# Kernel tuning notes

Measured on AMD Instinct MI355X. Metric: run time of the kernel, lower is better.

## Reference

```python
import jax, jax.numpy as jnp
import numpy as np

N, M, CIN, COUT, K, KS = 200000, 100000, 32, 64, 32, 3


def setup_inputs() -> dict:
    key = jax.random.key(0)
    ks = jax.random.split(key, 6)
    inp_positions = jax.random.uniform(ks[0], (N, 3), dtype=jnp.float32)
    out_positions = jax.random.uniform(ks[1], (M, 3), dtype=jnp.float32)
    inp_features = jax.random.normal(ks[2], (N, CIN), dtype=jnp.float32)
    inp_importance = jnp.ones((N,), dtype=jnp.float32)
    neighbors_index = jax.random.randint(ks[3], (M, K), 0, N, dtype=jnp.int32)
    kernel = 0.05 * jax.random.normal(ks[4], (KS, KS, KS, CIN, COUT), dtype=jnp.float32)
    bias = jnp.zeros((COUT,), dtype=jnp.float32)
    extents = jnp.ones((1,), dtype=jnp.float32)
    return dict(inp_features=inp_features, inp_positions=inp_positions,
                out_positions=out_positions, extents=extents,
                inp_importance=inp_importance, neighbors_index=neighbors_index,
                kernel=kernel, bias=bias)


def _axis_weights(x):
    """x: [...,] coord clamped to [0, KS-1]. Returns [..., KS] linear interp weights."""
    grid = jnp.arange(KS, dtype=x.dtype)
    return jnp.maximum(0.0, 1.0 - jnp.abs(x[..., None] - grid))


def reference(inp_features, inp_positions, out_positions, extents,
              inp_importance, neighbors_index, kernel, bias):
    radius = 0.5 * extents[0]
    nbr_pos = inp_positions[neighbors_index]                   # [M,K,3]
    rel = (nbr_pos - out_positions[:, None, :]) / radius       # unit-ball coords
    dist = jnp.sqrt(jnp.sum(rel * rel, axis=-1))               # [M,K] L2 metric
    mask = (dist <= 1.0).astype(inp_features.dtype)            # in-radius validity
    # ball_to_cube_radial: scale radially so sphere boundary -> cube boundary
    linf = jnp.max(jnp.abs(rel), axis=-1)                      # [M,K]
    scale = jnp.where(linf > 1e-8, dist / jnp.maximum(linf, 1e-8), 0.0)
    cube = rel * scale[..., None]                              # in [-1,1]^3
    # align_corners=True: map [-1,1] to voxel-center coords [0, KS-1]
    coords = jnp.clip((cube + 1.0) * (0.5 * (KS - 1)), 0.0, KS - 1.0)  # 'linear' clamp
    wx = _axis_weights(coords[..., 0])                         # [M,K,3]
    wy = _axis_weights(coords[..., 1])
    wz = _axis_weights(coords[..., 2])
    imp = mask * inp_importance[neighbors_index]               # [M,K]
    feat = inp_features[neighbors_index] * imp[..., None]      # [M,K,CIN]
    # accumulate importance*interp-weighted features per filter voxel
    acc = jnp.einsum('mka,mkb,mkc,mki->mabci', wx, wy, wz, feat)  # [M,3,3,3,CIN]
    out = jnp.einsum('mabci,abcio->mo', acc, kernel)           # [M,COUT]
    # normalize=True, no window fn -> divide by (importance-weighted) neighbor count
    norm = jnp.sum(imp, axis=1)                                # [M]
    out = out * jnp.where(norm > 0, 1.0 / jnp.maximum(norm, 1e-12), 0.0)[:, None]
    return out + bias  # activation=None
```

## Files before the change

### kernel.cpp

```cpp
#include <hip/hip_runtime.h>


typedef __attribute__((ext_vector_type(8))) __bf16 bf16x8;
typedef __attribute__((ext_vector_type(4))) __bf16 bf16x4;
typedef __attribute__((ext_vector_type(4))) float f32x4;
typedef unsigned int u32;
typedef unsigned short u16;

constexpr int NPTS = 200000;
constexpr int MPTS = 100000;
constexpr int MB   = 16;
constexpr int NBLK = MPTS / MB;

constexpr int PT_STRIDE = 2256;
constexpr int W_V       = 80;
constexpr int NRM_OFF   = MB * PT_STRIDE;
constexpr int LDS_BYTES = NRM_OFF + 64 + 256;

constexpr size_t WFRAG_ELEMS = 4 * 28 * 64 * 8;
constexpr size_t FEATS_OFF_ELEMS = WFRAG_ELEMS;
constexpr size_t WS_NEED = (WFRAG_ELEMS + (size_t)NPTS * 32) * 2;

__global__ void prep_kernel(const float* __restrict__ kern,
                            const float* __restrict__ feats,
                            __bf16* __restrict__ wsb) {
    const int blk = blockIdx.x;
    if (blk < 224) {
        const int tid = blk * 256 + threadIdx.x;
        const int j  = tid & 7;
        const int l  = (tid >> 3) & 63;
        const int s  = tid >> 9;
        const int ks = s % 28;
        const int nt = s / 28;
        const int kk = ks * 32 + ((l >> 4) << 3) + j;
        const int ch = kk / 28;
        const int v  = kk - ch * 28;
        const int o  = nt * 16 + (l & 15);
        const float val = (v < 27) ? kern[v * 2048 + ch * 64 + o] : 0.0f;
        wsb[tid] = (__bf16)val;
    } else {
        const int t = (blk - 224) * 256 + threadIdx.x;
        const float4* src = (const float4*)feats + (size_t)t * 2;
        const float4 a = src[0];
        const float4 b = src[1];
        bf16x8 o;
        o[0]=(__bf16)a.x; o[1]=(__bf16)a.y; o[2]=(__bf16)a.z; o[3]=(__bf16)a.w;
        o[4]=(__bf16)b.x; o[5]=(__bf16)b.y; o[6]=(__bf16)b.z; o[7]=(__bf16)b.w;
        *(bf16x8*)(wsb + FEATS_OFF_ELEMS + (size_t)t * 8) = o;
    }
}

#define STAGE(q) do {                                                       \
    const int4 nA = *(const int4*)(nb_base + (q) * 32);                     \
    const int4 nB = *(const int4*)(nb_base + (q) * 32 + 4);                 \
    if constexpr (PRE) {                                                    \
        stq[q][0] = featsb[(size_t)nA.x * 16 + lr];                         \
        stq[q][1] = featsb[(size_t)nA.y * 16 + lr];                         \
        stq[q][2] = featsb[(size_t)nA.z * 16 + lr];                         \
        stq[q][3] = featsb[(size_t)nA.w * 16 + lr];                         \
        stq[q][4] = featsb[(size_t)nB.x * 16 + lr];                         \
        stq[q][5] = featsb[(size_t)nB.y * 16 + lr];                         \
        stq[q][6] = featsb[(size_t)nB.z * 16 + lr];                         \
        stq[q][7] = featsb[(size_t)nB.w * 16 + lr];                         \
    } else {                                                                \
        stf[q][0] = ((const float2*)(feats + (size_t)nA.x * 32))[lr];       \
        stf[q][1] = ((const float2*)(feats + (size_t)nA.y * 32))[lr];       \
        stf[q][2] = ((const float2*)(feats + (size_t)nA.z * 32))[lr];       \
        stf[q][3] = ((const float2*)(feats + (size_t)nA.w * 32))[lr];       \
        stf[q][4] = ((const float2*)(feats + (size_t)nB.x * 32))[lr];       \
        stf[q][5] = ((const float2*)(feats + (size_t)nB.y * 32))[lr];       \
        stf[q][6] = ((const float2*)(feats + (size_t)nB.z * 32))[lr];       \
        stf[q][7] = ((const float2*)(feats + (size_t)nB.w * 32))[lr];       \
    }                                                                       \
} while (0)

#define COMPUTE(q) do {                                                     \
    unsigned char* pbase = smem + (wv * 4 + (q)) * PT_STRIDE;               \
    bf16x8 b0, b1;                                                          \
    if constexpr (PRE) {                                                    \
        union { u16 u[8]; bf16x8 v; } B0, B1;                               \
        _Pragma("unroll")                                                   \
        for (int j = 0; j < 8; ++j) {                                       \
            B0.u[j] = (u16)(stq[q][j] & 0xffffu);                           \
            B1.u[j] = (u16)(stq[q][j] >> 16);                               \
        }                                                                   \
        b0 = B0.v; b1 = B1.v;                                               \
    } else {                                                                \
        _Pragma("unroll")                                                   \
        for (int j = 0; j < 8; ++j) {                                       \
            b0[j] = (__bf16)stf[q][j].x;                                    \
            b1[j] = (__bf16)stf[q][j].y;                                    \
        }                                                                   \
    }                                                                       \
    const bf16x8 a0 = *(const bf16x8*)(pbase + lr * W_V + k0 * 2);          \
    const bf16x8 a1 = *(const bf16x8*)(pbase + (16 + lr) * W_V + k0 * 2);   \
    f32x4 d00 = {0.f,0.f,0.f,0.f}, d01 = {0.f,0.f,0.f,0.f};                 \
    f32x4 d10 = {0.f,0.f,0.f,0.f}, d11 = {0.f,0.f,0.f,0.f};                 \
    d00 = __builtin_amdgcn_mfma_f32_16x16x32_bf16(a0, b0, d00, 0, 0, 0);    \
    d01 = __builtin_amdgcn_mfma_f32_16x16x32_bf16(a0, b1, d01, 0, 0, 0);    \
    d10 = __builtin_amdgcn_mfma_f32_16x16x32_bf16(a1, b0, d10, 0, 0, 0);    \
    d11 = __builtin_amdgcn_mfma_f32_16x16x32_bf16(a1, b1, d11, 0, 0, 0);    \
    const int vb0 = grp * 4, vb1 = 16 + grp * 4;                            \
    const int ch0 = 2 * lr, ch1 = 2 * lr + 1;                               \
    bf16x4 t0, t1;                                                          \
    t0[0]=(__bf16)d00[0]; t0[1]=(__bf16)d00[1];                             \
    t0[2]=(__bf16)d00[2]; t0[3]=(__bf16)d00[3];                             \
    *(bf16x4*)(pbase + (ch0 * 28 + vb0) * 2) = t0;                          \
    t1[0]=(__bf16)d01[0]; t1[1]=(__bf16)d01[1];                             \
    t1[2]=(__bf16)d01[2]; t1[3]=(__bf16)d01[3];                             \
    *(bf16x4*)(pbase + (ch1 * 28 + vb0) * 2) = t1;                          \
    if (vb1 < 28) {                                                         \
        bf16x4 t2, t3;                                                      \
        t2[0]=(__bf16)d10[0]; t2[1]=(__bf16)d10[1];                         \
        t2[2]=(__bf16)d10[2]; t2[3]=(__bf16)d10[3];                         \
        *(bf16x4*)(pbase + (ch0 * 28 + vb1) * 2) = t2;                      \
        t3[0]=(__bf16)d11[0]; t3[1]=(__bf16)d11[1];                         \
        t3[2]=(__bf16)d11[2]; t3[3]=(__bf16)d11[3];                         \
        *(bf16x4*)(pbase + (ch1 * 28 + vb1) * 2) = t3;                      \
    }                                                                       \
} while (0)

template<bool PRE>
__global__ __launch_bounds__(256, 4)
void cconv_kernel(const float* __restrict__ feats,
                  const u32* __restrict__ featsb,
                  const float* __restrict__ inpos,
                  const float* __restrict__ outpos,
                  const float* __restrict__ extents,
                  const float* __restrict__ importance,
                  const int*   __restrict__ nbrs,
                  const __bf16* __restrict__ wfrag,
                  const float* __restrict__ bias,
                  float* __restrict__ out)
{
    __shared__ __align__(16) unsigned char smem[LDS_BYTES];

    const int tid = threadIdx.x;
    const int blk = blockIdx.x;
    float* nrm = (float*)(smem + NRM_OFF);

    const float inv_r = 2.0f / extents[0];

    {
        const int pt = tid >> 4;
        const int kp = tid & 15;
        const int m  = blk * MB + pt;
        const int2 nn = *(const int2*)(nbrs + m * 32 + 2 * kp);
        const float ox = outpos[3 * m + 0];
        const float oy = outpos[3 * m + 1];
        const float oz = outpos[3 * m + 2];

        float cxA, cyA, czA, impA, cxB, cyB, czB, impB;
        {
            const int nb = nn.x;
            const float rx = (inpos[3 * nb + 0] - ox) * inv_r;
            const float ry = (inpos[3 * nb + 1] - oy) * inv_r;
            const float rz = (inpos[3 * nb + 2] - oz) * inv_r;
            const float dist = sqrtf(rx * rx + ry * ry + rz * rz);
            float imp = importance[nb];
            impA = (dist <= 1.0f) ? imp : 0.0f;
            const float linf = fmaxf(fabsf(rx), fmaxf(fabsf(ry), fabsf(rz)));
            const float sc = (linf > 1e-8f) ? (dist / linf) : 0.0f;
            cxA = fminf(fmaxf(rx * sc + 1.0f, 0.0f), 2.0f);
            cyA = fminf(fmaxf(ry * sc + 1.0f, 0.0f), 2.0f);
            czA = fminf(fmaxf(rz * sc + 1.0f, 0.0f), 2.0f);
        }
        {
            const int nb = nn.y;
            const float rx = (inpos[3 * nb + 0] - ox) * inv_r;
            const float ry = (inpos[3 * nb + 1] - oy) * inv_r;
            const float rz = (inpos[3 * nb + 2] - oz) * inv_r;
            const float dist = sqrtf(rx * rx + ry * ry + rz * rz);
            float imp = importance[nb];
            impB = (dist <= 1.0f) ? imp : 0.0f;
            const float linf = fmaxf(fabsf(rx), fmaxf(fabsf(ry), fabsf(rz)));
            const float sc = (linf > 1e-8f) ? (dist / linf) : 0.0f;
            cxB = fminf(fmaxf(rx * sc + 1.0f, 0.0f), 2.0f);
            cyB = fminf(fmaxf(ry * sc + 1.0f, 0.0f), 2.0f);
            czB = fminf(fmaxf(rz * sc + 1.0f, 0.0f), 2.0f);
        }

        float wxA[3], wyA[3], wzA[3], wxB[3], wyB[3], wzB[3];
        wxA[0] = fmaxf(0.f, 1.f - cxA) * impA;
        wxA[1] = (1.f - fabsf(cxA - 1.f)) * impA;
        wxA[2] = fmaxf(0.f, cxA - 1.f) * impA;
        wyA[0] = fmaxf(0.f, 1.f - cyA); wyA[1] = 1.f - fabsf(cyA - 1.f); wyA[2] = fmaxf(0.f, cyA - 1.f);
        wzA[0] = fmaxf(0.f, 1.f - czA); wzA[1] = 1.f - fabsf(czA - 1.f); wzA[2] = fmaxf(0.f, czA - 1.f);
        wxB[0] = fmaxf(0.f, 1.f - cxB) * impB;
        wxB[1] = (1.f - fabsf(cxB - 1.f)) * impB;
        wxB[2] = fmaxf(0.f, cxB - 1.f) * impB;
        wyB[0] = fmaxf(0.f, 1.f - cyB); wyB[1] = 1.f - fabsf(cyB - 1.f); wyB[2] = fmaxf(0.f, cyB - 1.f);
        wzB[0] = fmaxf(0.f, 1.f - czB); wzB[1] = 1.f - fabsf(czB - 1.f); wzB[2] = fmaxf(0.f, czB - 1.f);

        unsigned char* wrow = smem + pt * PT_STRIDE + kp * 4;
#pragma unroll
        for (int a = 0; a < 3; ++a)
#pragma unroll
            for (int b = 0; b < 3; ++b) {
                const float pA = wxA[a] * wyA[b];
                const float pB = wxB[a] * wyB[b];
#pragma unroll
                for (int c = 0; c < 3; ++c) {
                    const int v = a * 9 + b * 3 + c;
                    union { __bf16 h[2]; u32 u; } pk;
                    pk.h[0] = (__bf16)(pA * wzA[c]);
                    pk.h[1] = (__bf16)(pB * wzB[c]);
                    *(u32*)(wrow + v * W_V) = pk.u;
                }
            }
        *(u32*)(wrow + 27 * W_V) = 0u;

        float s = impA + impB;
        s += __shfl_xor(s, 1);
        s += __shfl_xor(s, 2);
        s += __shfl_xor(s, 4);
        s += __shfl_xor(s, 8);
        if (kp == 0) nrm[pt] = (s > 0.f) ? (1.f / fmaxf(s, 1e-12f)) : 0.f;
    }

    const int wv   = tid >> 6;
    const int lane = tid & 63;
    const int grp  = lane >> 4;
    const int lr   = lane & 15;
    const int k0   = grp * 8;
    const int* nb_base = nbrs + (blk * MB + wv * 4) * 32 + k0;

    u32    stq[4][8];
    float2 stf[4][8];
    STAGE(0); STAGE(1); STAGE(2); STAGE(3);
    COMPUTE(0); COMPUTE(1); COMPUTE(2); COMPUTE(3);

    const bf16x8* wb = (const bf16x8*)wfrag;
    bf16x8 w0 = wb[(size_t)(wv * 28 + 0) * 64 + lane];
    bf16x8 w1 = wb[(size_t)(wv * 28 + 1) * 64 + lane];
    __syncthreads();

    const unsigned char* abase = smem + lr * PT_STRIDE + grp * 16;
    f32x4 e = {0.f, 0.f, 0.f, 0.f};
    bf16x8 a = *(const bf16x8*)(abase);
#pragma unroll
    for (int ks = 0; ks < 28; ++ks) {
        bf16x8 wn, an;
        if (ks < 26) wn = wb[(size_t)(wv * 28 + ks + 2) * 64 + lane];
        if (ks < 27) an = *(const bf16x8*)(abase + (ks + 1) * 64);
        e = __builtin_amdgcn_mfma_f32_16x16x32_bf16(a, w0, e, 0, 0, 0);
        w0 = w1;
        if (ks < 26) w1 = wn;
        if (ks < 27) a = an;
    }

    const int o  = wv * 16 + lr;
    const float bb = bias[o];
#pragma unroll
    for (int r = 0; r < 4; ++r) {
        const int pt = grp * 4 + r;
        out[(size_t)(blk * MB + pt) * 64 + o] = e[r] * nrm[pt] + bb;
    }
}

extern "C" void kernel_launch(void* const* d_in, const int* in_sizes, int n_in,
                              void* d_out, int out_size, void* d_ws, size_t ws_size,
                              hipStream_t stream) {
    (void)in_sizes; (void)n_in; (void)out_size;
    const float* feats      = (const float*)d_in[0];
    const float* inpos      = (const float*)d_in[1];
    const float* outpos     = (const float*)d_in[2];
    const float* extents    = (const float*)d_in[3];
    const float* importance = (const float*)d_in[4];
    const int*   nbrs       = (const int*)d_in[5];
    const float* kern       = (const float*)d_in[6];
    const float* bias       = (const float*)d_in[7];
    float* outp = (float*)d_out;
    __bf16* wsb = (__bf16*)d_ws;

    const bool pre = ws_size >= WS_NEED;

    hipLaunchKernelGGL(prep_kernel, dim3(pre ? 3349 : 224), dim3(256), 0, stream,
                       kern, feats, wsb);
    if (pre) {
        hipLaunchKernelGGL(cconv_kernel<true>, dim3(NBLK), dim3(256), 0, stream,
                           feats, (const u32*)(wsb + FEATS_OFF_ELEMS), inpos, outpos,
                           extents, importance, nbrs, wsb, bias, outp);
    } else {
        hipLaunchKernelGGL(cconv_kernel<false>, dim3(NBLK), dim3(256), 0, stream,
                           feats, (const u32*)(wsb + FEATS_OFF_ELEMS), inpos, outpos,
                           extents, importance, nbrs, wsb, bias, outp);
    }
}
```

Measured before the change: 189.7 us.

## Overlap feature gathers with weight phase, shrink and swizzle LDS, deepen MFMA prefetch

Result: no change. 192.5 us (+1.5%).

```diff
diff --git a/kernel.cpp b/kernel.cpp
--- a/kernel.cpp
+++ b/kernel.cpp
@@ -12,10 +12,10 @@
 constexpr int MB   = 16;
 constexpr int NBLK = MPTS / MB;
 
-constexpr int PT_STRIDE = 2256;
-constexpr int W_V       = 80;
+constexpr int W_V       = 72;
+constexpr int PT_STRIDE = 2016;
 constexpr int NRM_OFF   = MB * PT_STRIDE;
-constexpr int LDS_BYTES = NRM_OFF + 64 + 256;
+constexpr int LDS_BYTES = NRM_OFF + 64;
 
 constexpr size_t WFRAG_ELEMS = 4 * 28 * 64 * 8;
 constexpr size_t FEATS_OFF_ELEMS = WFRAG_ELEMS;
@@ -50,212 +50,245 @@
     }
 }
 
-#define STAGE(q) do {                                                       \
+__device__ __forceinline__ void phase0_weights(
+    unsigned char* smem, float* nrm, int blk, int tid,
+    const float* __restrict__ inpos, const float* __restrict__ outpos,
+    const float* __restrict__ importance, const int* __restrict__ nbrs,
+    float inv_r)
+{
+    const int pt = tid >> 4;
+    const int kp = tid & 15;
+    const int m  = blk * MB + pt;
+    const int2 nn = *(const int2*)(nbrs + m * 32 + 2 * kp);
+    const float ox = outpos[3 * m + 0];
+    const float oy = outpos[3 * m + 1];
+    const float oz = outpos[3 * m + 2];
+
+    float cxA, cyA, czA, impA, cxB, cyB, czB, impB;
+    {
+        const int nb = nn.x;
+        const float rx = (inpos[3 * nb + 0] - ox) * inv_r;
+        const float ry = (inpos[3 * nb + 1] - oy) * inv_r;
+        const float rz = (inpos[3 * nb + 2] - oz) * inv_r;
+        const float dist = sqrtf(rx * rx + ry * ry + rz * rz);
+        float imp = importance[nb];
+        impA = (dist <= 1.0f) ? imp : 0.0f;
+        const float linf = fmaxf(fabsf(rx), fmaxf(fabsf(ry), fabsf(rz)));
+        const float sc = (linf > 1e-8f) ? (dist / linf) : 0.0f;
+        cxA = fminf(fmaxf(rx * sc + 1.0f, 0.0f), 2.0f);
+        cyA = fminf(fmaxf(ry * sc + 1.0f, 0.0f), 2.0f);
+        czA = fminf(fmaxf(rz * sc + 1.0f, 0.0f), 2.0f);
+    }
+    {
+        const int nb = nn.y;
+        const float rx = (inpos[3 * nb + 0] - ox) * inv_r;
+        const float ry = (inpos[3 * nb + 1] - oy) * inv_r;
+        const float rz = (inpos[3 * nb + 2] - oz) * inv_r;
+        const float dist = sqrtf(rx * rx + ry * ry + rz * rz);
+        float imp = importance[nb];
+        impB = (dist <= 1.0f) ? imp : 0.0f;
+        const float linf = fmaxf(fabsf(rx), fmaxf(fabsf(ry), fabsf(rz)));
+        const float sc = (linf > 1e-8f) ? (dist / linf) : 0.0f;
+        cxB = fminf(fmaxf(rx * sc + 1.0f, 0.0f), 2.0f);
+        cyB = fminf(fmaxf(ry * sc + 1.0f, 0.0f), 2.0f);
+        czB = fminf(fmaxf(rz * sc + 1.0f, 0.0f), 2.0f);
+    }
+
+    float wxA[3], wyA[3], wzA[3], wxB[3], wyB[3], wzB[3];
+    wxA[0] = fmaxf(0.f, 1.f - cxA) * impA;
+    wxA[1] = (1.f - fabsf(cxA - 1.f)) * impA;
+    wxA[2] = fmaxf(0.f, cxA - 1.f) * impA;
+    wyA[0] = fmaxf(0.f, 1.f - cyA); wyA[1] = 1.f - fabsf(cyA - 1.f); wyA[2] = fmaxf(0.f, cyA - 1.f);
+    wzA[0] = fmaxf(0.f, 1.f - czA); wzA[1] = 1.f - fabsf(czA - 1.f); wzA[2] = fmaxf(0.f, czA - 1.f);
+    wxB[0] = fmaxf(0.f, 1.f - cxB) * impB;
+    wxB[1] = (1.f - fabsf(cxB - 1.f)) * impB;
+    wxB[2] = fmaxf(0.f, cxB - 1.f) * impB;
+    wyB[0] = fmaxf(0.f, 1.f - cyB); wyB[1] = 1.f - fabsf(cyB - 1.f); wyB[2] = fmaxf(0.f, cyB - 1.f);
+    wzB[0] = fmaxf(0.f, 1.f - czB); wzB[1] = 1.f - fabsf(czB - 1.f); wzB[2] = fmaxf(0.f, czB - 1.f);
+
+    unsigned char* wrow = smem + pt * PT_STRIDE + kp * 4;
+#pragma unroll
+    for (int a = 0; a < 3; ++a)
+#pragma unroll
+        for (int b = 0; b < 3; ++b) {
+            const float pA = wxA[a] * wyA[b];
+            const float pB = wxB[a] * wyB[b];
+#pragma unroll
+            for (int c = 0; c < 3; ++c) {
+                const int v = a * 9 + b * 3 + c;
+                union { __bf16 h[2]; u32 u; } pk;
+                pk.h[0] = (__bf16)(pA * wzA[c]);
+                pk.h[1] = (__bf16)(pB * wzB[c]);
+                *(u32*)(wrow + v * W_V) = pk.u;
+            }
+        }
+    *(u32*)(wrow + 27 * W_V) = 0u;
+
+    float s = impA + impB;
+    s += __shfl_xor(s, 1);
+    s += __shfl_xor(s, 2);
+    s += __shfl_xor(s, 4);
+    s += __shfl_xor(s, 8);
+    if (kp == 0) nrm[pt] = (s > 0.f) ? (1.f / fmaxf(s, 1e-12f)) : 0.f;
+}
+
+__device__ __forceinline__ void compute_pt(
+    unsigned char* smem, int ptq, int lr, int grp, bf16x8 b0, bf16x8 b1)
+{
+    unsigned char* pbase = smem + ptq * PT_STRIDE;
+    const u32 sw = ((u32)(ptq & 7)) << 4;
+    const bf16x8 a0 = *(const bf16x8*)(pbase + lr * W_V + grp * 16);
+    const int rr = (16 + lr > 27) ? 27 : (16 + lr);
+    const bf16x8 a1 = *(const bf16x8*)(pbase + rr * W_V + grp * 16);
+
+    f32x4 d00 = {0.f,0.f,0.f,0.f}, d01 = {0.f,0.f,0.f,0.f};
+    f32x4 d10 = {0.f,0.f,0.f,0.f}, d11 = {0.f,0.f,0.f,0.f};
+    d00 = __builtin_amdgcn_mfma_f32_16x16x32_bf16(a0, b0, d00, 0, 0, 0);
+    d01 = __builtin_amdgcn_mfma_f32_16x16x32_bf16(a0, b1, d01, 0, 0, 0);
+    d10 = __builtin_amdgcn_mfma_f32_16x16x32_bf16(a1, b0, d10, 0, 0, 0);
+    d11 = __builtin_amdgcn_mfma_f32_16x16x32_bf16(a1, b1, d11, 0, 0, 0);
+
+    const int vb0 = grp * 4, vb1 = 16 + grp * 4;
+    bf16x4 t;
+    t[0]=(__bf16)d00[0]; t[1]=(__bf16)d00[1]; t[2]=(__bf16)d00[2]; t[3]=(__bf16)d00[3];
+    *(bf16x4*)(pbase + (((u32)(112 * lr + 2 * vb0)) ^ sw)) = t;
+    t[0]=(__bf16)d01[0]; t[1]=(__bf16)d01[1]; t[2]=(__bf16)d01[2]; t[3]=(__bf16)d01[3];
+    *(bf16x4*)(pbase + (((u32)(112 * lr + 56 + 2 * vb0)) ^ sw)) = t;
+    if (vb1 < 28) {
+        t[0]=(__bf16)d10[0]; t[1]=(__bf16)d10[1]; t[2]=(__bf16)d10[2]; t[3]=(__bf16)d10[3];
+        *(bf16x4*)(pbase + (((u32)(112 * lr + 2 * vb1)) ^ sw)) = t;
+        t[0]=(__bf16)d11[0]; t[1]=(__bf16)d11[1]; t[2]=(__bf16)d11[2]; t[3]=(__bf16)d11[3];
+        *(bf16x4*)(pbase + (((u32)(112 * lr + 56 + 2 * vb1)) ^ sw)) = t;
+    }
+}
+
+#define SQ(q) do {                                                          \
     const int4 nA = *(const int4*)(nb_base + (q) * 32);                     \
     const int4 nB = *(const int4*)(nb_base + (q) * 32 + 4);                 \
-    if constexpr (PRE) {                                                    \
-        stq[q][0] = featsb[(size_t)nA.x * 16 + lr];                         \
-        stq[q][1] = featsb[(size_t)nA.y * 16 + lr];                         \
-        stq[q][2] = featsb[(size_t)nA.z * 16 + lr];                         \
-        stq[q][3] = featsb[(size_t)nA.w * 16 + lr];                         \
-        stq[q][4] = featsb[(size_t)nB.x * 16 + lr];                         \
-        stq[q][5] = featsb[(size_t)nB.y * 16 + lr];                         \
-        stq[q][6] = featsb[(size_t)nB.z * 16 + lr];                         \
-        stq[q][7] = featsb[(size_t)nB.w * 16 + lr];                         \
-    } else {                                                                \
-        stf[q][0] = ((const float2*)(feats + (size_t)nA.x * 32))[lr];       \
-        stf[q][1] = ((const float2*)(feats + (size_t)nA.y * 32))[lr];       \
-        stf[q][2] = ((const float2*)(feats + (size_t)nA.z * 32))[lr];       \
-        stf[q][3] = ((const float2*)(feats + (size_t)nA.w * 32))[lr];       \
-        stf[q][4] = ((const float2*)(feats + (size_t)nB.x * 32))[lr];       \
-        stf[q][5] = ((const float2*)(feats + (size_t)nB.y * 32))[lr];       \
-        stf[q][6] = ((const float2*)(feats + (size_t)nB.z * 32))[lr];       \
-        stf[q][7] = ((const float2*)(feats + (size_t)nB.w * 32))[lr];       \
+    stq[q][0] = featsb[(size_t)nA.x * 16 + lr];                             \
+    stq[q][1] = featsb[(size_t)nA.y * 16 + lr];                             \
+    stq[q][2] = featsb[(size_t)nA.z * 16 + lr];                             \
+    stq[q][3] = featsb[(size_t)nA.w * 16 + lr];                             \
+    stq[q][4] = featsb[(size_t)nB.x * 16 + lr];                             \
+    stq[q][5] = featsb[(size_t)nB.y * 16 + lr];                             \
+    stq[q][6] = featsb[(size_t)nB.z * 16 + lr];                             \
+    stq[q][7] = featsb[(size_t)nB.w * 16 + lr];                             \
+} while (0)
+
+#define CQ(q) do {                                                          \
+    union { u16 u[8]; bf16x8 v; } B0, B1;                                   \
+    _Pragma("unroll")                                                       \
+    for (int j = 0; j < 8; ++j) {                                           \
+        B0.u[j] = (u16)(stq[q][j] & 0xffffu);                               \
+        B1.u[j] = (u16)(stq[q][j] >> 16);                                   \
     }                                                                       \
+    compute_pt(smem, wv * 4 + (q), lr, grp, B0.v, B1.v);                    \
 } while (0)
 
-#define COMPUTE(q) do {                                                     \
-    unsigned char* pbase = smem + (wv * 4 + (q)) * PT_STRIDE;               \
+#define SF(q, b) do {                                                       \
+    const int4 nA = *(const int4*)(nb_base + (q) * 32);                     \
+    const int4 nB = *(const int4*)(nb_base + (q) * 32 + 4);                 \
+    stf[b][0] = ((const float2*)(feats + (size_t)nA.x * 32))[lr];           \
+    stf[b][1] = ((const float2*)(feats + (size_t)nA.y * 32))[lr];           \
+    stf[b][2] = ((const float2*)(feats + (size_t)nA.z * 32))[lr];           \
+    stf[b][3] = ((const float2*)(feats + (size_t)nA.w * 32))[lr];           \
+    stf[b][4] = ((const float2*)(feats + (size_t)nB.x * 32))[lr];           \
+    stf[b][5] = ((const float2*)(feats + (size_t)nB.y * 32))[lr];           \
+    stf[b][6] = ((const float2*)(feats + (size_t)nB.z * 32))[lr];           \
+    stf[b][7] = ((const float2*)(feats + (size_t)nB.w * 32))[lr];           \
+} while (0)
+
+#define CF(q, b) do {                                                       \
     bf16x8 b0, b1;                                                          \
-    if constexpr (PRE) {                                                    \
-        union { u16 u[8]; bf16x8 v; } B0, B1;                               \
-        _Pragma("unroll")                                                   \
-        for (int j = 0; j < 8; ++j) {                                       \
-            B0.u[j] = (u16)(stq[q][j] & 0xffffu);                           \
-            B1.u[j] = (u16)(stq[q][j] >> 16);                               \
-        }                                                                   \
-        b0 = B0.v; b1 = B1.v;                                               \
-    } else {                                                                \
-        _Pragma("unroll")                                                   \
-        for (int j = 0; j < 8; ++j) {                                       \
-            b0[j] = (__bf16)stf[q][j].x;                                    \
-            b1[j] = (__bf16)stf[q][j].y;                                    \
-        }                                                                   \
+    _Pragma("unroll")                                                       \
+    for (int j = 0; j < 8; ++j) {                                           \
+        b0[j] = (__bf16)stf[b][j].x;                                        \
+        b1[j] = (__bf16)stf[b][j].y;                                        \
     }                                                                       \
-    const bf16x8 a0 = *(const bf16x8*)(pbase + lr * W_V + k0 * 2);          \
-    const bf16x8 a1 = *(const bf16x8*)(pbase + (16 + lr) * W_V + k0 * 2);   \
-    f32x4 d00 = {0.f,0.f,0.f,0.f}, d01 = {0.f,0.f,0.f,0.f};                 \
-    f32x4 d10 = {0.f,0.f,0.f,0.f}, d11 = {0.f,0.f,0.f,0.f};                 \
-    d00 = __builtin_amdgcn_mfma_f32_16x16x32_bf16(a0, b0, d00, 0, 0, 0);    \
-    d01 = __builtin_amdgcn_mfma_f32_16x16x32_bf16(a0, b1, d01, 0, 0, 0);    \
-    d10 = __builtin_amdgcn_mfma_f32_16x16x32_bf16(a1, b0, d10, 0, 0, 0);    \
-    d11 = __builtin_amdgcn_mfma_f32_16x16x32_bf16(a1, b1, d11, 0, 0, 0);    \
-    const int vb0 = grp * 4, vb1 = 16 + grp * 4;                            \
-    const int ch0 = 2 * lr, ch1 = 2 * lr + 1;                               \
-    bf16x4 t0, t1;                                                          \
-    t0[0]=(__bf16)d00[0]; t0[1]=(__bf16)d00[1];                             \
-    t0[2]=(__bf16)d00[2]; t0[3]=(__bf16)d00[3];                             \
-    *(bf16x4*)(pbase + (ch0 * 28 + vb0) * 2) = t0;                          \
-    t1[0]=(__bf16)d01[0]; t1[1]=(__bf16)d01[1];                             \
-    t1[2]=(__bf16)d01[2]; t1[3]=(__bf16)d01[3];                             \
-    *(bf16x4*)(pbase + (ch1 * 28 + vb0) * 2) = t1;                          \
-    if (vb1 < 28) {                                                         \
-        bf16x4 t2, t3;                                                      \
-        t2[0]=(__bf16)d10[0]; t2[1]=(__bf16)d10[1];                         \
-        t2[2]=(__bf16)d10[2]; t2[3]=(__bf16)d10[3];                         \
-        *(bf16x4*)(pbase + (ch0 * 28 + vb1) * 2) = t2;                      \
-        t3[0]=(__bf16)d11[0]; t3[1]=(__bf16)d11[1];                         \
-        t3[2]=(__bf16)d11[2]; t3[3]=(__bf16)d11[3];                         \
-        *(bf16x4*)(pbase + (ch1 * 28 + vb1) * 2) = t3;                      \
-    }                                                                       \
+    compute_pt(smem, wv * 4 + (q), lr, grp, b0, b1);                        \
 } while (0)
 
-template<bool PRE>
-__global__ __launch_bounds__(256, 4)
-void cconv_kernel(const float* __restrict__ feats,
-                  const u32* __restrict__ featsb,
-                  const float* __restrict__ inpos,
-                  const float* __restrict__ outpos,
-                  const float* __restrict__ extents,
-                  const float* __restrict__ importance,
-                  const int*   __restrict__ nbrs,
-                  const __bf16* __restrict__ wfrag,
-                  const float* __restrict__ bias,
-                  float* __restrict__ out)
+template<int PRE>
+__device__ __forceinline__ void cconv_impl(
+    const float* __restrict__ feats, const u32* __restrict__ featsb,
+    const float* __restrict__ inpos, const float* __restrict__ outpos,
+    const float* __restrict__ extents, const float* __restrict__ importance,
+    const int* __restrict__ nbrs, const __bf16* __restrict__ wfrag,
+    const float* __restrict__ bias, float* __restrict__ out)
 {
     __shared__ __align__(16) unsigned char smem[LDS_BYTES];
-
     const int tid = threadIdx.x;
     const int blk = blockIdx.x;
     float* nrm = (float*)(smem + NRM_OFF);
-
     const float inv_r = 2.0f / extents[0];
 
-    {
-        const int pt = tid >> 4;
-        const int kp = tid & 15;
-        const int m  = blk * MB + pt;
-        const int2 nn = *(const int2*)(nbrs + m * 32 + 2 * kp);
-        const float ox = outpos[3 * m + 0];
-        const float oy = outpos[3 * m + 1];
-        const float oz = outpos[3 * m + 2];
-
-        float cxA, cyA, czA, impA, cxB, cyB, czB, impB;
-        {
-            const int nb = nn.x;
-            const float rx = (inpos[3 * nb + 0] - ox) * inv_r;
-            const float ry = (inpos[3 * nb + 1] - oy) * inv_r;
-            const float rz = (inpos[3 * nb + 2] - oz) * inv_r;
-            const float dist = sqrtf(rx * rx + ry * ry + rz * rz);
-            float imp = importance[nb];
-            impA = (dist <= 1.0f) ? imp : 0.0f;
-            const float linf = fmaxf(fabsf(rx), fmaxf(fabsf(ry), fabsf(rz)));
-            const float sc = (linf > 1e-8f) ? (dist / linf) : 0.0f;
-            cxA = fminf(fmaxf(rx * sc + 1.0f, 0.0f), 2.0f);
-            cyA = fminf(fmaxf(ry * sc + 1.0f, 0.0f), 2.0f);
-            czA = fminf(fmaxf(rz * sc + 1.0f, 0.0f), 2.0f);
+    const int wv = tid >> 6, lane = tid & 63, grp = lane >> 4, lr = lane & 15;
+    const int* nb_base = nbrs + (blk * MB + wv * 4) * 32 + grp * 8;
+
+    if constexpr (PRE) {
+        u32 stq[4][8];
+        SQ(0); SQ(1);
+        phase0_weights(smem, nrm, blk, tid, inpos, outpos, importance, nbrs, inv_r);
+        SQ(2); SQ(3);
+        CQ(0); CQ(1); CQ(2); CQ(3);
+    } else {
+        phase0_weights(smem, nrm, blk, tid, inpos, outpos, importance, nbrs, inv_r);
+        float2 stf[2][8];
+        SF(0, 0); SF(1, 1);
+        CF(0, 0); SF(2, 0);
+        CF(1, 1); SF(3, 1);
+        CF(2, 0); CF(3, 1);
+    }
+
+    const bf16x8* wb = (const bf16x8*)wfrag;
+    const size_t wvb = (size_t)(wv * 28) * 64 + lane;
+    bf16x8 wreg[4];
+    wreg[0] = wb[wvb];       wreg[1] = wb[wvb + 64];
+    wreg[2] = wb[wvb + 128]; wreg[3] = wb[wvb + 192];
+    __syncthreads();
+
+    const unsigned char* abase = smem + lr * PT_STRIDE;
+    const u32 swr = ((u32)(lr & 7)) << 4;
+    bf16x8 areg[4];
+#pragma unroll
+    for (int i = 0; i < 4; ++i)
+        areg[i] = *(const bf16x8*)(abase + (((u32)(i * 64 + grp * 16)) ^ swr));
+
+    f32x4 e = {0.f, 0.f, 0.f, 0.f};
+#pragma unroll
+    for (int ks = 0; ks < 28; ++ks) {
+        e = __builtin_amdgcn_mfma_f32_16x16x32_bf16(areg[ks & 3], wreg[ks & 3], e, 0, 0, 0);
+        if (ks + 4 < 28) {
+            wreg[ks & 3] = wb[wvb + (size_t)(ks + 4) * 64];
+            areg[ks & 3] = *(const bf16x8*)(abase + (((u32)((ks + 4) * 64 + grp * 16)) ^ swr));
         }
-        {
-            const int nb = nn.y;
-            const float rx = (inpos[3 * nb + 0] - ox) * inv_r;
-            const float ry = (inpos[3 * nb + 1] - oy) * inv_r;
-            const float rz = (inpos[3 * nb + 2] - oz) * inv_r;
-            const float dist = sqrtf(rx * rx + ry * ry + rz * rz);
-            float imp = importance[nb];
-            impB = (dist <= 1.0f) ? imp : 0.0f;
-            const float linf = fmaxf(fabsf(rx), fmaxf(fabsf(ry), fabsf(rz)));
-            const float sc = (linf > 1e-8f) ? (dist / linf) : 0.0f;
-            cxB = fminf(fmaxf(rx * sc + 1.0f, 0.0f), 2.0f);
-            cyB = fminf(fmaxf(ry * sc + 1.0f, 0.0f), 2.0f);
-            czB = fminf(fmaxf(rz * sc + 1.0f, 0.0f), 2.0f);
-        }
-
-        float wxA[3], wyA[3], wzA[3], wxB[3], wyB[3], wzB[3];
-        wxA[0] = fmaxf(0.f, 1.f - cxA) * impA;
-        wxA[1] = (1.f - fabsf(cxA - 1.f)) * impA;
-        wxA[2] = fmaxf(0.f, cxA - 1.f) * impA;
-        wyA[0] = fmaxf(0.f, 1.f - cyA); wyA[1] = 1.f - fabsf(cyA - 1.f); wyA[2] = fmaxf(0.f, cyA - 1.f);
-        wzA[0] = fmaxf(0.f, 1.f - czA); wzA[1] = 1.f - fabsf(czA - 1.f); wzA[2] = fmaxf(0.f, czA - 1.f);
-        wxB[0] = fmaxf(0.f, 1.f - cxB) * impB;
-        wxB[1] = (1.f - fabsf(cxB - 1.f)) * impB;
-        wxB[2] = fmaxf(0.f, cxB - 1.f) * impB;
-        wyB[0] = fmaxf(0.f, 1.f - cyB); wyB[1] = 1.f - fabsf(cyB - 1.f); wyB[2] = fmaxf(0.f, cyB - 1.f);
-        wzB[0] = fmaxf(0.f, 1.f - czB); wzB[1] = 1.f - fabsf(czB - 1.f); wzB[2] = fmaxf(0.f, czB - 1.f);
-
-        unsigned char* wrow = smem + pt * PT_STRIDE + kp * 4;
-#pragma unroll
-        for (int a = 0; a < 3; ++a)
-#pragma unroll
-            for (int b = 0; b < 3; ++b) {
-                const float pA = wxA[a] * wyA[b];
-                const float pB = wxB[a] * wyB[b];
-#pragma unroll
-                for (int c = 0; c < 3; ++c) {
-                    const int v = a * 9 + b * 3 + c;
-                    union { __bf16 h[2]; u32 u; } pk;
-                    pk.h[0] = (__bf16)(pA * wzA[c]);
-                    pk.h[1] = (__bf16)(pB * wzB[c]);
-                    *(u32*)(wrow + v * W_V) = pk.u;
-                }
-            }
-        *(u32*)(wrow + 27 * W_V) = 0u;
-
-        float s = impA + impB;
-        s += __shfl_xor(s, 1);
-        s += __shfl_xor(s, 2);
-        s += __shfl_xor(s, 4);
-        s += __shfl_xor(s, 8);
-        if (kp == 0) nrm[pt] = (s > 0.f) ? (1.f / fmaxf(s, 1e-12f)) : 0.f;
-    }
-
-    const int wv   = tid >> 6;
-    const int lane = tid & 63;
-    const int grp  = lane >> 4;
-    const int lr   = lane & 15;
-    const int k0   = grp * 8;
-    const int* nb_base = nbrs + (blk * MB + wv * 4) * 32 + k0;
-
-    u32    stq[4][8];
-    float2 stf[4][8];
-    STAGE(0); STAGE(1); STAGE(2); STAGE(3);
-    COMPUTE(0); COMPUTE(1); COMPUTE(2); COMPUTE(3);
-
-    const bf16x8* wb = (const bf16x8*)wfrag;
-    bf16x8 w0 = wb[(size_t)(wv * 28 + 0) * 64 + lane];
-    bf16x8 w1 = wb[(size_t)(wv * 28 + 1) * 64 + lane];
-    __syncthreads();
-
-    const unsigned char* abase = smem + lr * PT_STRIDE + grp * 16;
-    f32x4 e = {0.f, 0.f, 0.f, 0.f};
-    bf16x8 a = *(const bf16x8*)(abase);
-#pragma unroll
-    for (int ks = 0; ks < 28; ++ks) {
-        bf16x8 wn, an;
-        if (ks < 26) wn = wb[(size_t)(wv * 28 + ks + 2) * 64 + lane];
-        if (ks < 27) an = *(const bf16x8*)(abase + (ks + 1) * 64);
-        e = __builtin_amdgcn_mfma_f32_16x16x32_bf16(a, w0, e, 0, 0, 0);
-        w0 = w1;
-        if (ks < 26) w1 = wn;
-        if (ks < 27) a = an;
-    }
-
-    const int o  = wv * 16 + lr;
+    }
+
+    const int o = wv * 16 + lr;
     const float bb = bias[o];
 #pragma unroll
     for (int r = 0; r < 4; ++r) {
         const int pt = grp * 4 + r;
         out[(size_t)(blk * MB + pt) * 64 + o] = e[r] * nrm[pt] + bb;
     }
+}
+
+__global__ __launch_bounds__(256, 5)
+void cconv_pre(const float* __restrict__ feats, const u32* __restrict__ featsb,
+               const float* __restrict__ inpos, const float* __restrict__ outpos,
+               const float* __restrict__ extents, const float* __restrict__ importance,
+               const int* __restrict__ nbrs, const __bf16* __restrict__ wfrag,
+               const float* __restrict__ bias, float* __restrict__ out) {
+    cconv_impl<1>(feats, featsb, inpos, outpos, extents, importance, nbrs, wfrag, bias, out);
+}
+
+__global__ __launch_bounds__(256, 5)
+void cconv_f32(const float* __restrict__ feats, const u32* __restrict__ featsb,
+               const float* __restrict__ inpos, const float* __restrict__ outpos,
+               const float* __restrict__ extents, const float* __restrict__ importance,
+               const int* __restrict__ nbrs, const __bf16* __restrict__ wfrag,
+               const float* __restrict__ bias, float* __restrict__ out) {
+    cconv_impl<0>(feats, featsb, inpos, outpos, extents, importance, nbrs, wfrag, bias, out);
 }
 
 extern "C" void kernel_launch(void* const* d_in, const int* in_sizes, int n_in,
@@ -272,18 +305,19 @@
     const float* bias       = (const float*)d_in[7];
     float* outp = (float*)d_out;
     __bf16* wsb = (__bf16*)d_ws;
+    const u32* featsb = (const u32*)(wsb + FEATS_OFF_ELEMS);
 
     const bool pre = ws_size >= WS_NEED;
 
     hipLaunchKernelGGL(prep_kernel, dim3(pre ? 3349 : 224), dim3(256), 0, stream,
                        kern, feats, wsb);
     if (pre) {
-        hipLaunchKernelGGL(cconv_kernel<true>, dim3(NBLK), dim3(256), 0, stream,
-                           feats, (const u32*)(wsb + FEATS_OFF_ELEMS), inpos, outpos,
-                           extents, importance, nbrs, wsb, bias, outp);
+        hipLaunchKernelGGL(cconv_pre, dim3(NBLK), dim3(256), 0, stream,
+                           feats, featsb, inpos, outpos, extents, importance,
+                           nbrs, wsb, bias, outp);
     } else {
-        hipLaunchKernelGGL(cconv_kernel<false>, dim3(NBLK), dim3(256), 0, stream,
-                           feats, (const u32*)(wsb + FEATS_OFF_ELEMS), inpos, outpos,
-                           extents, importance, nbrs, wsb, bias, outp);
-    }
-}
+        hipLaunchKernelGGL(cconv_f32, dim3(NBLK), dim3(256), 0, stream,
+                           feats, featsb, inpos, outpos, extents, importance,
+                           nbrs, wsb, bias, outp);
+    }
+}
```
